# Optimization experiments

Hardware: AMD Instinct MI355X
Metric: run time of the kernel (lower is better)

Reference implementation:

```python
import jax, jax.numpy as jnp
import numpy as np

NUM_IN, NUM_OUT, SD, BATCH = 2048, 8192, 5, 4096
INIT_DELTA = 0.01


def _dist(a, b):
    # a: [I,1,D], b: [1,O,D] -> [I,O]
    return jnp.sqrt(jnp.sum((a - b) ** 2, axis=-1))


def setup_inputs() -> dict:
    key = jax.random.key(0)
    k1, k2, k3, k4, k5 = jax.random.split(key, 5)
    init_in_pos = jax.random.normal(k1, (NUM_IN, 1, SD), dtype=jnp.float32)
    init_out_pos = jax.random.normal(k2, (1, NUM_OUT, SD), dtype=jnp.float32)
    in_pos = init_in_pos + INIT_DELTA * jax.random.normal(k3, (NUM_IN, 1, SD), dtype=jnp.float32)
    out_pos = init_out_pos + INIT_DELTA * jax.random.normal(k4, (1, NUM_OUT, SD), dtype=jnp.float32)
    inputs = jax.random.normal(k5, (BATCH, NUM_IN), dtype=jnp.float32)
    biases = jnp.zeros((NUM_OUT,), dtype=jnp.float32)
    return {"inputs": inputs, "init_in_pos": init_in_pos, "init_out_pos": init_out_pos,
            "in_pos": in_pos, "out_pos": out_pos, "biases": biases}


def reference(inputs, init_in_pos, init_out_pos, in_pos, out_pos, biases):
    # weight = ||in_pos - out_pos|| - ||init_in_pos - init_out_pos||, shape [I,O]
    w = _dist(in_pos, out_pos) - _dist(init_in_pos, init_out_pos)
    return inputs @ w + biases
```

## Files before the change

### kernel.cpp

```cpp
#include <hip/hip_runtime.h>
#include <hip/hip_bf16.h>
#include <stdint.h>

#define NUM_IN  2048
#define NUM_OUT 8192
#define BATCH   4096
#define SD      5

#define BM 256
#define BN 256
#define BK 32
#define NT (NUM_IN / BK)
#define TILEE (BM * BK)

typedef __bf16 bf16x8 __attribute__((ext_vector_type(8)));
typedef float  f32x4  __attribute__((ext_vector_type(4)));
typedef unsigned short ushort_t;
typedef ushort_t ushort8 __attribute__((ext_vector_type(8)));

static __device__ __forceinline__ ushort_t bf16_bits(float f) {
  __hip_bfloat16 h = __float2bfloat16(f);
  ushort_t u;
  __builtin_memcpy(&u, &h, 2);
  return u;
}

__global__ __launch_bounds__(256) void cvt_kernel(const float* __restrict__ x,
                                                  ushort_t* __restrict__ y) {
  const int i = (blockIdx.x * 256 + threadIdx.x) * 8;
  float4 v0 = *reinterpret_cast<const float4*>(x + i);
  float4 v1 = *reinterpret_cast<const float4*>(x + i + 4);
  ushort8 o;
  o[0] = bf16_bits(v0.x); o[1] = bf16_bits(v0.y);
  o[2] = bf16_bits(v0.z); o[3] = bf16_bits(v0.w);
  o[4] = bf16_bits(v1.x); o[5] = bf16_bits(v1.y);
  o[6] = bf16_bits(v1.z); o[7] = bf16_bits(v1.w);
  *reinterpret_cast<ushort8*>(y + i) = o;
}

__global__ __launch_bounds__(256) void genw_kernel(
    const float* __restrict__ in_pos, const float* __restrict__ out_pos,
    const float* __restrict__ init_in, const float* __restrict__ init_out,
    ushort_t* __restrict__ Wt) {
  __shared__ float s_ip[NUM_IN * SD];
  __shared__ float s_iip[NUM_IN * SD];
  const int tid = threadIdx.x;
#pragma unroll
  for (int i = 0; i < 10; ++i) {
    const int idx = i * 1024 + tid * 4;
    *reinterpret_cast<float4*>(&s_ip[idx]) =
        *reinterpret_cast<const float4*>(in_pos + idx);
    *reinterpret_cast<float4*>(&s_iip[idx]) =
        *reinterpret_cast<const float4*>(init_in + idx);
  }
  __syncthreads();

  const int n  = blockIdx.x * 16 + (tid >> 4);
  const int kg = tid & 15;
  float op[SD], iop[SD];
#pragma unroll
  for (int d = 0; d < SD; ++d) {
    op[d]  = out_pos[n * SD + d];
    iop[d] = init_out[n * SD + d];
  }
#pragma unroll 1
  for (int kb = 0; kb < 16; ++kb) {
    const int k0 = kb * 128 + kg * 8;
    float buf[40], ibuf[40];
#pragma unroll
    for (int j = 0; j < 10; ++j) {
      float4 v = *reinterpret_cast<const float4*>(&s_ip[k0 * SD + j * 4]);
      buf[4 * j + 0] = v.x; buf[4 * j + 1] = v.y;
      buf[4 * j + 2] = v.z; buf[4 * j + 3] = v.w;
      float4 u = *reinterpret_cast<const float4*>(&s_iip[k0 * SD + j * 4]);
      ibuf[4 * j + 0] = u.x; ibuf[4 * j + 1] = u.y;
      ibuf[4 * j + 2] = u.z; ibuf[4 * j + 3] = u.w;
    }
    ushort8 o;
#pragma unroll
    for (int i = 0; i < 8; ++i) {
      float d1 = 0.f, d0 = 0.f;
#pragma unroll
      for (int d = 0; d < SD; ++d) {
        float a = buf[i * SD + d] - op[d];
        float b = ibuf[i * SD + d] - iop[d];
        d1 += a * a;
        d0 += b * b;
      }
      o[i] = bf16_bits(sqrtf(d1) - sqrtf(d0));
    }
    *reinterpret_cast<ushort8*>(Wt + (size_t)n * NUM_IN + k0) = o;
  }
}

__global__ __launch_bounds__(512, 1) void gemm_kernel(
    const ushort_t* __restrict__ A,
    const ushort_t* __restrict__ Bt,
    const float* __restrict__ bias,
    float* __restrict__ C) {
  __shared__ __align__(16) ushort_t sA[4 * TILEE];
  __shared__ __align__(16) ushort_t sB[4 * TILEE];

  const int tid  = threadIdx.x;
  const int w    = tid >> 6;
  const int l    = tid & 63;
  const int wm   = w >> 2;
  const int wn   = w & 3;
  const int lrow = l & 15;
  const int lkc  = l >> 4;

  const int orig = blockIdx.x;
  const int lin  = (orig & 7) * 64 + (orig >> 3);
  const int bx   = lin >> 4;
  const int by   = lin & 15;
  const int m0   = by * BM;
  const int n0   = bx * BN;

  const int phys  = ((4 * (lrow & 1) + lkc) ^ (lrow >> 1));
  const int laneo = (lrow >> 1) * 64 + phys * 8;
  const int AbW = wm * 4096;
  const int BbW = wn * 2048;

  const int cc  = (tid & 7) ^ ((tid >> 3) & 7);
  const int row = 2 * (tid >> 3) + (cc >> 2);
  const int ke  = (cc & 3) * 8;
  const ushort_t* pA0 = A  + (size_t)(m0 + row) * NUM_IN + ke;
  const ushort_t* pA1 = A  + (size_t)(m0 + row + 128) * NUM_IN + ke;
  const ushort_t* pB0 = Bt + (size_t)(n0 + row) * NUM_IN + ke;
  const ushort_t* pB1 = Bt + (size_t)(n0 + row + 128) * NUM_IN + ke;

#define GLDS(src, dst)                                                         \
  __builtin_amdgcn_global_load_lds(                                            \
      reinterpret_cast<const __attribute__((address_space(1))) uint32_t*>(     \
          (uintptr_t)(src)),                                                   \
      reinterpret_cast<__attribute__((address_space(3))) uint32_t*>(           \
          (uintptr_t)(dst)),                                                   \
      16, 0, 0)

#define STAGE(bs, kt)                                                          \
  {                                                                            \
    GLDS(pA0 + (kt), &sA[(bs) * TILEE + tid * 8]);                             \
    GLDS(pA1 + (kt), &sA[(bs) * TILEE + tid * 8 + 4096]);                      \
    GLDS(pB0 + (kt), &sB[(bs) * TILEE + tid * 8]);                             \
    GLDS(pB1 + (kt), &sB[(bs) * TILEE + tid * 8 + 4096]);                      \
  }

#define RD_A(arr, bs, mh)                                                      \
  {                                                                            \
    _Pragma("unroll")                                                          \
    for (int mi = 0; mi < 4; ++mi)                                             \
      arr[mi] = *reinterpret_cast<const bf16x8*>(                              \
          &sA[(bs) * TILEE + AbW + (mh) * 2048 + mi * 512 + laneo]);           \
  }
#define RD_B(arr, bs, nh)                                                      \
  {                                                                            \
    _Pragma("unroll")                                                          \
    for (int nj = 0; nj < 2; ++nj)                                             \
      arr[nj] = *reinterpret_cast<const bf16x8*>(                              \
          &sB[(bs) * TILEE + BbW + (nh) * 1024 + nj * 512 + laneo]);           \
  }

#define MFMA8(mh, nh, Aa, Bx)                                                  \
  {                                                                            \
    __builtin_amdgcn_s_setprio(1);                                             \
    _Pragma("unroll")                                                          \
    for (int mi = 0; mi < 4; ++mi)                                             \
      _Pragma("unroll")                                                        \
      for (int nj = 0; nj < 2; ++nj)                                           \
        acc[(mh) * 4 + mi][(nh) * 2 + nj] =                                    \
            __builtin_amdgcn_mfma_f32_16x16x32_bf16(                           \
                Aa[mi], Bx[nj], acc[(mh) * 4 + mi][(nh) * 2 + nj], 0, 0, 0);   \
    __builtin_amdgcn_s_setprio(0);                                             \
  }

#define LGKM(n)  asm volatile("s_waitcnt lgkmcnt(" #n ")" ::: "memory")
#define SCHED0   __builtin_amdgcn_sched_barrier(0)
#define BARRIER  __builtin_amdgcn_s_barrier()
#define VMCNT4   asm volatile("s_waitcnt vmcnt(4)" ::: "memory")
#define VMCNT0   asm volatile("s_waitcnt vmcnt(0)" ::: "memory")

#define KTILE(CUR, NXT, ktn)                                                   \
  {                                                                            \
    STAGE(NXT, ktn)                                                            \
    RD_A(aE, CUR, 0) RD_B(b0, CUR, 0)                                          \
    RD_B(b1, CUR, 1)                                                           \
    LGKM(2); SCHED0;                                                           \
    MFMA8(0, 0, aE, b0)                                                        \
    RD_A(aO, CUR, 1)                                                           \
    LGKM(4); SCHED0;                                                           \
    MFMA8(0, 1, aE, b1)                                                        \
    LGKM(0); SCHED0;                                                           \
    MFMA8(1, 0, aO, b0)                                                        \
    MFMA8(1, 1, aO, b1)                                                        \
    VMCNT4;                                                                    \
    BARRIER;                                                                   \
  }

  f32x4 acc[8][4];
#pragma unroll
  for (int i = 0; i < 8; ++i)
#pragma unroll
    for (int j = 0; j < 4; ++j) acc[i][j] = f32x4{0.f, 0.f, 0.f, 0.f};

  bf16x8 aE[4], aO[4], b0[2], b1[2];

  STAGE(0, 0)
  STAGE(1, BK)
  VMCNT4;
  BARRIER;

#pragma unroll 1
  for (int tt = 0; tt < NT; tt += 4) {
    const int k2 = (tt + 2 < NT ? tt + 2 : NT - 1) * BK;
    const int k3 = (tt + 3 < NT ? tt + 3 : NT - 1) * BK;
    const int k4 = (tt + 4 < NT ? tt + 4 : NT - 1) * BK;
    const int k5 = (tt + 5 < NT ? tt + 5 : NT - 1) * BK;
    KTILE(0, 2, k2)
    KTILE(1, 3, k3)
    KTILE(2, 0, k4)
    KTILE(3, 1, k5)
  }

  const int er = l >> 4;
  const int ec = l & 15;
#pragma unroll
  for (int nh = 0; nh < 2; ++nh) {
#pragma unroll
    for (int nj = 0; nj < 2; ++nj) {
      const int col = n0 + wn * 64 + nh * 32 + nj * 16 + ec;
      const float bi = bias[col];
#pragma unroll
      for (int mh = 0; mh < 2; ++mh) {
#pragma unroll
        for (int mi = 0; mi < 4; ++mi) {
#pragma unroll
          for (int j = 0; j < 4; ++j) {
            const int row = m0 + wm * 128 + mh * 64 + mi * 16 + er * 4 + j;
            C[(size_t)row * NUM_OUT + col] =
                acc[mh * 4 + mi][nh * 2 + nj][j] + bi;
          }
        }
      }
    }
  }
#undef KTILE
#undef STAGE
#undef RD_A
#undef RD_B
#undef MFMA8
#undef GLDS
}

extern "C" void kernel_launch(void* const* d_in, const int* in_sizes, int n_in,
                              void* d_out, int out_size, void* d_ws, size_t ws_size,
                              hipStream_t stream) {
  const float* inputs   = (const float*)d_in[0];
  const float* init_in  = (const float*)d_in[1];
  const float* init_out = (const float*)d_in[2];
  const float* in_pos   = (const float*)d_in[3];
  const float* out_pos  = (const float*)d_in[4];
  const float* biases   = (const float*)d_in[5];
  float* out = (float*)d_out;

  ushort_t* Abf = (ushort_t*)d_ws;
  ushort_t* Wt  = (ushort_t*)((char*)d_ws + (size_t)BATCH * NUM_IN * 2);

  cvt_kernel<<<(BATCH * NUM_IN) / (256 * 8), 256, 0, stream>>>(inputs, Abf);
  genw_kernel<<<NUM_OUT / 16, 256, 0, stream>>>(
      in_pos, out_pos, init_in, init_out, Wt);
  gemm_kernel<<<(BATCH / BM) * (NUM_OUT / BN), 512, 0, stream>>>(
      Abf, Wt, biases, out);
}
```

Measured before the change: 169.2 us.

## Pair K-tiles into windows with one barrier and early LDS fragment prefetch

Measured after the change: 171.8 us. About the same (+1.5%).

```diff
diff --git a/kernel.cpp b/kernel.cpp
--- a/kernel.cpp
+++ b/kernel.cpp
@@ -176,24 +176,36 @@
 #define LGKM(n)  asm volatile("s_waitcnt lgkmcnt(" #n ")" ::: "memory")
 #define SCHED0   __builtin_amdgcn_sched_barrier(0)
 #define BARRIER  __builtin_amdgcn_s_barrier()
-#define VMCNT4   asm volatile("s_waitcnt vmcnt(4)" ::: "memory")
 #define VMCNT0   asm volatile("s_waitcnt vmcnt(0)" ::: "memory")
 
-#define KTILE(CUR, NXT, ktn)                                                   \
-  {                                                                            \
-    STAGE(NXT, ktn)                                                            \
-    RD_A(aE, CUR, 0) RD_B(b0, CUR, 0)                                          \
-    RD_B(b1, CUR, 1)                                                           \
+#define WINDOW(CA, CB, kA2, kB2, NA)                                           \
+  {                                                                            \
+                                                \
+    STAGE(CA ^ 2, kA2)                                                         \
+    RD_B(b1, CA, 1)                                           \
+    LGKM(2); SCHED0;                                          \
+    MFMA8(0, 0, aE, b0)                                                        \
+    RD_A(aO, CA, 1)                                                  \
+    LGKM(4); SCHED0;                                             \
+    MFMA8(0, 1, aE, b1)                                                        \
+    LGKM(0); SCHED0;                                             \
+    MFMA8(1, 0, aO, b0)                                                        \
+    RD_A(aE, CB, 0) RD_B(b0, CB, 0)    \
+    MFMA8(1, 1, aO, b1)                                                        \
+                                                \
+    STAGE(CB ^ 2, kB2)                                                         \
+    RD_B(b1, CB, 1)                                                            \
     LGKM(2); SCHED0;                                                           \
     MFMA8(0, 0, aE, b0)                                                        \
-    RD_A(aO, CUR, 1)                                                           \
+    RD_A(aO, CB, 1)                                                            \
     LGKM(4); SCHED0;                                                           \
     MFMA8(0, 1, aE, b1)                                                        \
     LGKM(0); SCHED0;                                                           \
     MFMA8(1, 0, aO, b0)                                                        \
+    VMCNT0;                              \
+    BARRIER;                                 \
+    RD_A(aE, NA, 0) RD_B(b0, NA, 0)        \
     MFMA8(1, 1, aO, b1)                                                        \
-    VMCNT4;                                                                    \
-    BARRIER;                                                                   \
   }
 
   f32x4 acc[8][4];
@@ -206,8 +218,9 @@
 
   STAGE(0, 0)
   STAGE(1, BK)
-  VMCNT4;
+  VMCNT0;
   BARRIER;
+  RD_A(aE, 0, 0) RD_B(b0, 0, 0)
 
 #pragma unroll 1
   for (int tt = 0; tt < NT; tt += 4) {
@@ -215,11 +228,10 @@
     const int k3 = (tt + 3 < NT ? tt + 3 : NT - 1) * BK;
     const int k4 = (tt + 4 < NT ? tt + 4 : NT - 1) * BK;
     const int k5 = (tt + 5 < NT ? tt + 5 : NT - 1) * BK;
-    KTILE(0, 2, k2)
-    KTILE(1, 3, k3)
-    KTILE(2, 0, k4)
-    KTILE(3, 1, k5)
-  }
+    WINDOW(0, 1, k2, k3, 2)
+    WINDOW(2, 3, k4, k5, 0)
+  }
+  asm volatile("s_waitcnt lgkmcnt(0)" ::: "memory");
 
   const int er = l >> 4;
   const int ec = l & 15;
@@ -243,7 +255,7 @@
       }
     }
   }
-#undef KTILE
+#undef WINDOW
 #undef STAGE
 #undef RD_A
 #undef RD_B
```
